# Kernel tuning notes

Measured on AMD Instinct MI355X. Metric: run time of the kernel, lower is better.

The kernel has to match this reference:

```python
import jax, jax.numpy as jnp
import numpy as np
from jax import lax

CONV3_NUM = 5
CONV1_NUM = 1
NEG_SLOPE = 0.2


def _leaky(x):
    return jnp.where(x >= 0, x, NEG_SLOPE * x)


def _per_sample_conv(x, k, b, pad):
    # x: [B,3,H,W], k: [B,3,3,kh,kw] (OIHW per sample), b: [B,3]
    def one(xi, ki, bi):
        y = lax.conv_general_dilated(
            xi[None], ki, (1, 1), ((pad, pad), (pad, pad)),
            dimension_numbers=("NCHW", "OIHW", "NCHW"))[0]
        return y + bi[:, None, None]
    return jax.vmap(one)(x, k, b)


def _conv3x3_block(x, feat):
    B = x.shape[0]
    k = feat[:, :81].reshape(B, 3, 3, 3, 3)
    b = feat[:, 81:84]
    return _leaky(x + _per_sample_conv(x, k, b, 1))


def _conv1x1_block(x, feat):
    B = x.shape[0]
    k = feat[:, :9].reshape(B, 3, 3, 1, 1)
    b = feat[:, 9:12]
    return _leaky(x + _per_sample_conv(x, k, b, 0))


def _att_map(f, h, w, xi):
    # f: [B,20]; h,w: [1,1,H,W]; xi: [B,1,H,W]  -> cubic trivariate polynomial
    c = lambda i: f[:, i][:, None, None, None]
    h2 = h * h; h3 = h2 * h
    w2 = w * w; w3 = w2 * w
    x2 = xi * xi; x3 = x2 * xi
    return (c(0) * h3 + c(1) * h2 * w + c(2) * h2 * xi + c(3) * h2
            + c(4) * h * w2 + c(5) * h * w * xi + c(6) * h * w
            + c(7) * h * x2 + c(8) * h * xi + c(9) * h
            + c(10) * w3 + c(11) * w2 * xi + c(12) * w2
            + c(13) * w * x2 + c(14) * w * xi + c(15) * w
            + c(16) * x3 + c(17) * x2 + c(18) * xi + c(19))


def setup_inputs() -> dict:
    key = jax.random.key(0)
    k1, k2, k3 = jax.random.split(key, 3)
    x = jax.random.normal(k1, (8, 3, 1024, 1024), dtype=jnp.float32)
    thumb_x = jax.random.normal(k2, (8, 3, 256, 256), dtype=jnp.float32)
    # meta() is an external CNN predicting per-sample params; we materialize its
    # output directly (scaled small for numerical stability of the conv stack).
    feature = jax.random.normal(k3, (8, 492), dtype=jnp.float32) * 0.05
    return {"x": x, "thumb_x": thumb_x, "feature": feature}


def reference(x, thumb_x, feature):
    B, _, H, W = x.shape
    residual = x
    for i in range(CONV3_NUM):
        x = _conv3x3_block(x, feature[:, i * 84:(i + 1) * 84])
    off = CONV3_NUM * 84
    for i in range(CONV1_NUM):
        x = _conv1x1_block(x, feature[:, off + i * 12:off + (i + 1) * 12])
    off = off + CONV1_NUM * 12
    x = residual + x
    dt = x.dtype
    h_mat = jnp.broadcast_to((jnp.arange(H, dtype=dt) / H)[None, None, :, None], (1, 1, H, W))
    w_mat = jnp.broadcast_to((jnp.arange(W, dtype=dt) / W)[None, None, None, :], (1, 1, H, W))
    atts = [_att_map(feature[:, off + 20 * c:off + 20 * (c + 1)], h_mat, w_mat, x[:, c:c + 1])
            for c in range(3)]
    att = jnp.concatenate(atts, axis=1)
    x = x * (1 + att)
    # location is None => thumbnail branch is skipped, thumb_x returned as-is
    return (x, thumb_x)
```

## Files before the change

kernel.cpp:

```cpp
#include <hip/hip_runtime.h>
#include <hip/hip_fp16.h>

typedef unsigned int uint;
typedef _Float16 h2 __attribute__((ext_vector_type(2)));


#define ROWS   42
#define W_U    26
#define W_REAL 23
#define CHP_U  (ROWS*W_U)
#define BUF_U  (3*CHP_U)

__device__ __forceinline__ h2   U2H(uint u) { return __builtin_bit_cast(h2, u); }
__device__ __forceinline__ uint H2U(h2 h)   { return __builtin_bit_cast(uint, h); }

__global__ void prep_weights(const float* __restrict__ feat, uint* __restrict__ wtab)
{
    const int b = blockIdx.x;
    const int t = threadIdx.x;
    float w = 0.f;
    bool valid = false;
    if (t < 405) {
        int l = t / 81, r = t % 81;
        int ic = r / 27; r %= 27;
        int ky = r / 9;  r %= 9;
        int oc = r / 3;
        int kx = r % 3;
        w = feat[b * 492 + l * 84 + ((oc * 3 + ic) * 3 + ky) * 3 + kx];
        valid = true;
    } else if (t < 420) {
        int i = t - 405;
        w = feat[b * 492 + (i / 3) * 84 + 81 + (i % 3)];
        valid = true;
    }
    if (valid) {
        _Float16 h = (_Float16)w;
        h2 hh = { h, h };
        wtab[b * 448 + t] = H2U(hh);
    }
}

__global__ __launch_bounds__(512, 8) void fused_net(
    const float* __restrict__ xin,
    const float* __restrict__ thumb,
    const float* __restrict__ feat,
    const uint*  __restrict__ wtab,
    float* __restrict__ out)
{
    const int tid = threadIdx.x;

    if (blockIdx.x == 32) {
        const int part = blockIdx.y + 32 * blockIdx.z;
        const float4* s4 = (const float4*)thumb;
        float4* d4 = (float4*)(out + 25165824ull);
        const int n4 = 1572864 / 4;
        for (int i = part * 512 + tid; i < n4; i += 256 * 512)
            d4[i] = s4[i];
        return;
    }

    const int gx0 = blockIdx.x * 32;
    const int gy0 = blockIdx.y * 32;
    const int b   = blockIdx.z;
    const bool edge = (gx0 == 0) | (gx0 == 992) | (gy0 == 0) | (gy0 == 992);
    const float* wf = feat + b * 492;
    const uint*  wt = wtab + b * 448;

    __shared__ uint lds[2 * BUF_U + 8];
    uint* b0 = lds;
    uint* b1 = lds + BUF_U + 4;

    const float* xb = xin + ((size_t)(b * 3) << 20);
    if (!edge) {
        for (int idx = tid; idx < 3 * ROWS * W_REAL; idx += 512) {
            int ch  = idx / (ROWS * W_REAL);
            int rem = idx - ch * (ROWS * W_REAL);
            int row = rem / W_REAL;
            int u   = rem - row * W_REAL;
            const float2 f = *(const float2*)(xb + ((size_t)ch << 20) +
                                              ((size_t)(gy0 - 5 + row) << 10) +
                                              (gx0 - 6 + 2 * u));
            b0[ch * CHP_U + row * W_U + u] =
                __builtin_bit_cast(uint, __builtin_amdgcn_cvt_pkrtz(f.x, f.y));
        }
    } else {
        for (int idx = tid; idx < 3 * ROWS * W_REAL; idx += 512) {
            int ch  = idx / (ROWS * W_REAL);
            int rem = idx - ch * (ROWS * W_REAL);
            int row = rem / W_REAL;
            int u   = rem - row * W_REAL;
            const int gy = gy0 - 5 + row;
            const int gx = gx0 - 6 + 2 * u;
            float2 f = {0.f, 0.f};
            if ((unsigned)gy < 1024u && (unsigned)gx < 1024u)
                f = *(const float2*)(xb + ((size_t)ch << 20) + ((size_t)gy << 10) + gx);
            b0[ch * CHP_U + row * W_U + u] =
                __builtin_bit_cast(uint, __builtin_amdgcn_cvt_pkrtz(f.x, f.y));
        }
    }
    __syncthreads();

    const int erow = tid >> 4;
    const int col2 = (tid & 15) << 1;
    const int ub   = (5 + erow) * W_U + 3 + (col2 >> 1);
    uint resu[3];
    #pragma unroll
    for (int ch = 0; ch < 3; ++ch) resu[ch] = b0[ch * CHP_U + ub];

    const h2 c02 = { (_Float16)0.2f, (_Float16)0.2f };

    #pragma unroll
    for (int l = 0; l < 5; ++l) {
        uint* sb = (l & 1) ? b1 : b0;
        uint* db = (l & 1) ? b0 : b1;
        const int S   = 40 - 2 * l;
        const int R   = S >> 1;
        const int xs  = (S + 3) >> 2;
        const int nst = R * xs;
        const int oy  = l + 1;
        const int EX  = (l + 2) & ~1;
        if (tid < nst) {
            const int r  = tid / xs;
            const int c  = tid - r * xs;
            const int y0 = oy + 2 * r;
            const int x0 = EX + 4 * c;
            const int bu = (x0 >> 1) - 1;

            h2 accA[2][3], accB[2][3];
            #pragma unroll
            for (int oc = 0; oc < 3; ++oc) {
                const h2 bi = U2H(wt[405 + l * 3 + oc]);
                accA[0][oc] = bi; accA[1][oc] = bi;
                accB[0][oc] = bi; accB[1][oc] = bi;
            }
            #pragma unroll
            for (int ic = 0; ic < 3; ++ic) {
                const int ai = ic * CHP_U + (y0 - 1) * W_U + bu;
                #pragma unroll
                for (int t = 0; t < 4; ++t) {
                    const int a = ai + t * W_U;
                    const uint u0 = sb[a], u1 = sb[a + 1], u2 = sb[a + 2], u3 = sb[a + 3];
                    const h2 X01 = U2H((u0 >> 16) | (u1 << 16));
                    const h2 C1  = U2H(u1);
                    const h2 X12 = U2H((u1 >> 16) | (u2 << 16));
                    const h2 C2  = U2H(u2);
                    const h2 X23 = U2H((u2 >> 16) | (u3 << 16));
                    #pragma unroll
                    for (int j = 0; j < 2; ++j) {
                        const int ky = t - j;
                        if (0 <= ky && ky <= 2) {
                            const int wb = l * 81 + (ic * 3 + ky) * 9;
                            #pragma unroll
                            for (int oc = 0; oc < 3; ++oc) {
                                const h2 w0 = U2H(wt[wb + oc * 3 + 0]);
                                const h2 w1 = U2H(wt[wb + oc * 3 + 1]);
                                const h2 w2 = U2H(wt[wb + oc * 3 + 2]);
                                accA[j][oc] = __builtin_elementwise_fma(w0, X01, accA[j][oc]);
                                accA[j][oc] = __builtin_elementwise_fma(w1, C1,  accA[j][oc]);
                                accA[j][oc] = __builtin_elementwise_fma(w2, X12, accA[j][oc]);
                                accB[j][oc] = __builtin_elementwise_fma(w0, X12, accB[j][oc]);
                                accB[j][oc] = __builtin_elementwise_fma(w1, C2,  accB[j][oc]);
                                accB[j][oc] = __builtin_elementwise_fma(w2, X23, accB[j][oc]);
                            }
                        }
                    }
                    if (t == 1) { accA[0][ic] += C1; accB[0][ic] += C2; }
                    if (t == 2) { accA[1][ic] += C1; accB[1][ic] += C2; }
                }
            }
            const int obase = y0 * W_U + (x0 >> 1);
            if (!edge) {
                #pragma unroll
                for (int j = 0; j < 2; ++j) {
                    #pragma unroll
                    for (int oc = 0; oc < 3; ++oc) {
                        h2 vA = accA[j][oc]; vA = __builtin_elementwise_max(vA, c02 * vA);
                        h2 vB = accB[j][oc]; vB = __builtin_elementwise_max(vB, c02 * vB);
                        db[oc * CHP_U + obase + j * W_U]     = H2U(vA);
                        db[oc * CHP_U + obase + j * W_U + 1] = H2U(vB);
                    }
                }
            } else {
                const int gy  = gy0 - 5 + y0;
                const int gxA = gx0 - 6 + x0;
                const uint mA0 = ((((unsigned)gxA       < 1024u) ? 0x0000ffffu : 0u) |
                                  (((unsigned)(gxA + 1) < 1024u) ? 0xffff0000u : 0u));
                const uint mB0 = ((((unsigned)(gxA + 2) < 1024u) ? 0x0000ffffu : 0u) |
                                  (((unsigned)(gxA + 3) < 1024u) ? 0xffff0000u : 0u));
                #pragma unroll
                for (int j = 0; j < 2; ++j) {
                    const uint mrow = ((unsigned)(gy + j) < 1024u) ? 0xffffffffu : 0u;
                    const uint mA = mrow & mA0, mB = mrow & mB0;
                    #pragma unroll
                    for (int oc = 0; oc < 3; ++oc) {
                        h2 vA = accA[j][oc]; vA = __builtin_elementwise_max(vA, c02 * vA);
                        h2 vB = accB[j][oc]; vB = __builtin_elementwise_max(vB, c02 * vB);
                        db[oc * CHP_U + obase + j * W_U]     = H2U(vA) & mA;
                        db[oc * CHP_U + obase + j * W_U + 1] = H2U(vB) & mB;
                    }
                }
            }
        }
        __syncthreads();
    }

    float x5f[3][2], resf[3][2];
    #pragma unroll
    for (int ch = 0; ch < 3; ++ch) {
        h2 hr = U2H(resu[ch]);
        resf[ch][0] = (float)hr.x; resf[ch][1] = (float)hr.y;
        h2 hx = U2H(b1[ch * CHP_U + ub]);
        x5f[ch][0] = (float)hx.x; x5f[ch][1] = (float)hx.y;
    }
    const int gy = gy0 + erow;
    const float h1 = (float)gy * (1.0f / 1024.0f);
    const float h2v = h1 * h1, h3 = h2v * h1;
    float* outb = out + ((size_t)(b * 3) << 20);
    float tmp[3][2];
    #pragma unroll
    for (int j = 0; j < 2; ++j) {
        const float wc = (float)(gx0 + col2 + j) * (1.0f / 1024.0f);
        const float w2 = wc * wc, w3 = w2 * wc;
        const float hw = h1 * wc, h2w = h2v * wc, hw2 = h1 * w2;
        #pragma unroll
        for (int oc = 0; oc < 3; ++oc) {
            float s = x5f[oc][j] + wf[429 + oc]
                    + wf[420 + oc * 3 + 0] * x5f[0][j]
                    + wf[420 + oc * 3 + 1] * x5f[1][j]
                    + wf[420 + oc * 3 + 2] * x5f[2][j];
            s = s >= 0.f ? s : 0.2f * s;
            const float xf = resf[oc][j] + s;
            const float x1 = xf, x2 = x1 * x1, x3 = x2 * x1;
            const float* cf = wf + 432 + oc * 20;
            float att =
                cf[0] * h3 + cf[1] * h2w + cf[2] * h2v * x1 + cf[3] * h2v +
                cf[4] * hw2 + cf[5] * hw * x1 + cf[6] * hw + cf[7] * h1 * x2 +
                cf[8] * h1 * x1 + cf[9] * h1 + cf[10] * w3 + cf[11] * w2 * x1 +
                cf[12] * w2 + cf[13] * wc * x2 + cf[14] * wc * x1 + cf[15] * wc +
                cf[16] * x3 + cf[17] * x2 + cf[18] * x1 + cf[19];
            tmp[oc][j] = xf * (1.f + att);
        }
    }
    #pragma unroll
    for (int oc = 0; oc < 3; ++oc) {
        float2 v = {tmp[oc][0], tmp[oc][1]};
        *(float2*)&outb[((size_t)oc << 20) + ((size_t)gy << 10) + (gx0 + col2)] = v;
    }
}

extern "C" void kernel_launch(void* const* d_in, const int* in_sizes, int n_in,
                              void* d_out, int out_size, void* d_ws, size_t ws_size,
                              hipStream_t stream) {
    const float* x     = (const float*)d_in[0];
    const float* thumb = (const float*)d_in[1];
    const float* feat  = (const float*)d_in[2];
    float* out = (float*)d_out;
    uint* wtab = (uint*)d_ws;

    prep_weights<<<dim3(8), 448, 0, stream>>>(feat, wtab);
    dim3 grid(33, 32, 8);
    fused_net<<<grid, 512, 0, stream>>>(x, thumb, feat, wtab, out);
}
```

Before: 301.4 us.

## Widen fused conv tile to 64 columns with fixed per-thread stencil mapping

Each block's output tile grows from 32x32 to 64 wide by 32 tall. The halo fraction per block falls, so less redundant halo compute and fewer global loads per output. Every layer now computes the full 40x72 region with a fixed thread-to-stencil mapping. LDS reads become 64-bit vector loads, and edge masks are computed once instead of branching per layer. The costs are a larger LDS footprint (occupancy hint lowered to 6), half as many blocks, and wasted computation on the shrinking interior region in later layers.

```diff
diff --git a/kernel.cpp b/kernel.cpp
--- a/kernel.cpp
+++ b/kernel.cpp
@@ -6,8 +6,8 @@
 
 
 #define ROWS   42
-#define W_U    26
-#define W_REAL 23
+#define W_U    42
+#define W_REAL 38
 #define CHP_U  (ROWS*W_U)
 #define BUF_U  (3*CHP_U)
 
@@ -40,7 +40,7 @@
     }
 }
 
-__global__ __launch_bounds__(512, 8) void fused_net(
+__global__ __launch_bounds__(512, 6) void fused_net(
     const float* __restrict__ xin,
     const float* __restrict__ thumb,
     const float* __restrict__ feat,
@@ -49,7 +49,7 @@
 {
     const int tid = threadIdx.x;
 
-    if (blockIdx.x == 32) {
+    if (blockIdx.x == 16) {
         const int part = blockIdx.y + 32 * blockIdx.z;
         const float4* s4 = (const float4*)thumb;
         float4* d4 = (float4*)(out + 25165824ull);
@@ -59,14 +59,14 @@
         return;
     }
 
-    const int gx0 = blockIdx.x * 32;
+    const int gx0 = blockIdx.x * 64;
     const int gy0 = blockIdx.y * 32;
     const int b   = blockIdx.z;
-    const bool edge = (gx0 == 0) | (gx0 == 992) | (gy0 == 0) | (gy0 == 992);
+    const bool edge = (gx0 == 0) | (gx0 == 960) | (gy0 == 0) | (gy0 == 992);
     const float* wf = feat + b * 492;
     const uint*  wt = wtab + b * 448;
 
-    __shared__ uint lds[2 * BUF_U + 8];
+    __shared__ __align__(16) uint lds[2 * BUF_U + 8];
     uint* b0 = lds;
     uint* b1 = lds + BUF_U + 4;
 
@@ -100,32 +100,46 @@
     }
     __syncthreads();
 
-    const int erow = tid >> 4;
-    const int col2 = (tid & 15) << 1;
-    const int ub   = (5 + erow) * W_U + 3 + (col2 >> 1);
-    uint resu[3];
+    const int er  = tid >> 5;
+    const int uc  = tid & 31;
+    const int ub0 = (5 + er) * W_U + 3 + uc;
+    const int ub1 = ub0 + 16 * W_U;
+    uint resu[2][3];
     #pragma unroll
-    for (int ch = 0; ch < 3; ++ch) resu[ch] = b0[ch * CHP_U + ub];
+    for (int ch = 0; ch < 3; ++ch) {
+        resu[0][ch] = b0[ch * CHP_U + ub0];
+        resu[1][ch] = b0[ch * CHP_U + ub1];
+    }
+
+    const int cr = tid / 18;
+    const int cc = tid - cr * 18;
+    const int y0 = 1 + 2 * cr;
+    const int x0 = 2 + 4 * cc;
+    uint mA[2] = {~0u, ~0u}, mB[2] = {~0u, ~0u};
+    if (edge) {
+        const int gyA = gy0 - 5 + y0;
+        const int gxA = gx0 - 6 + x0;
+        const uint mA0 = ((((unsigned)gxA       < 1024u) ? 0x0000ffffu : 0u) |
+                          (((unsigned)(gxA + 1) < 1024u) ? 0xffff0000u : 0u));
+        const uint mB0 = ((((unsigned)(gxA + 2) < 1024u) ? 0x0000ffffu : 0u) |
+                          (((unsigned)(gxA + 3) < 1024u) ? 0xffff0000u : 0u));
+        #pragma unroll
+        for (int j = 0; j < 2; ++j) {
+            const uint mr = ((unsigned)(gyA + j) < 1024u) ? ~0u : 0u;
+            mA[j] = mA0 & mr;
+            mB[j] = mB0 & mr;
+        }
+    }
 
     const h2 c02 = { (_Float16)0.2f, (_Float16)0.2f };
 
     #pragma unroll
     for (int l = 0; l < 5; ++l) {
-        uint* sb = (l & 1) ? b1 : b0;
-        uint* db = (l & 1) ? b0 : b1;
-        const int S   = 40 - 2 * l;
-        const int R   = S >> 1;
-        const int xs  = (S + 3) >> 2;
-        const int nst = R * xs;
-        const int oy  = l + 1;
-        const int EX  = (l + 2) & ~1;
-        if (tid < nst) {
-            const int r  = tid / xs;
-            const int c  = tid - r * xs;
-            const int y0 = oy + 2 * r;
-            const int x0 = EX + 4 * c;
-            const int bu = (x0 >> 1) - 1;
-
+        const uint* sb = (l & 1) ? b1 : b0;
+        uint*       db = (l & 1) ? b0 : b1;
+        if (tid < 360) {
+            const uint* tb = sb + (y0 - 1) * W_U + 2 * cc;
+            uint*       ob = db + y0 * W_U + 1 + 2 * cc;
             h2 accA[2][3], accB[2][3];
             #pragma unroll
             for (int oc = 0; oc < 3; ++oc) {
@@ -135,11 +149,11 @@
             }
             #pragma unroll
             for (int ic = 0; ic < 3; ++ic) {
-                const int ai = ic * CHP_U + (y0 - 1) * W_U + bu;
                 #pragma unroll
                 for (int t = 0; t < 4; ++t) {
-                    const int a = ai + t * W_U;
-                    const uint u0 = sb[a], u1 = sb[a + 1], u2 = sb[a + 2], u3 = sb[a + 3];
+                    const uint2 P = *(const uint2*)(tb + ic * CHP_U + t * W_U);
+                    const uint2 Q = *(const uint2*)(tb + ic * CHP_U + t * W_U + 2);
+                    const uint u0 = P.x, u1 = P.y, u2 = Q.x, u3 = Q.y;
                     const h2 X01 = U2H((u0 >> 16) | (u1 << 16));
                     const h2 C1  = U2H(u1);
                     const h2 X12 = U2H((u1 >> 16) | (u2 << 16));
@@ -164,87 +178,69 @@
                             }
                         }
                     }
-                    if (t == 1) { accA[0][ic] += C1; accB[0][ic] += C2; }
-                    if (t == 2) { accA[1][ic] += C1; accB[1][ic] += C2; }
+                    if (t == 1) { accA[0][ic] = accA[0][ic] + C1; accB[0][ic] = accB[0][ic] + C2; }
+                    if (t == 2) { accA[1][ic] = accA[1][ic] + C1; accB[1][ic] = accB[1][ic] + C2; }
                 }
             }
-            const int obase = y0 * W_U + (x0 >> 1);
-            if (!edge) {
+            #pragma unroll
+            for (int j = 0; j < 2; ++j) {
                 #pragma unroll
-                for (int j = 0; j < 2; ++j) {
-                    #pragma unroll
-                    for (int oc = 0; oc < 3; ++oc) {
-                        h2 vA = accA[j][oc]; vA = __builtin_elementwise_max(vA, c02 * vA);
-                        h2 vB = accB[j][oc]; vB = __builtin_elementwise_max(vB, c02 * vB);
-                        db[oc * CHP_U + obase + j * W_U]     = H2U(vA);
-                        db[oc * CHP_U + obase + j * W_U + 1] = H2U(vB);
-                    }
+                for (int oc = 0; oc < 3; ++oc) {
+                    h2 vA = accA[j][oc]; vA = __builtin_elementwise_max(vA, c02 * vA);
+                    h2 vB = accB[j][oc]; vB = __builtin_elementwise_max(vB, c02 * vB);
+                    ob[oc * CHP_U + j * W_U]     = H2U(vA) & mA[j];
+                    ob[oc * CHP_U + j * W_U + 1] = H2U(vB) & mB[j];
                 }
-            } else {
-                const int gy  = gy0 - 5 + y0;
-                const int gxA = gx0 - 6 + x0;
-                const uint mA0 = ((((unsigned)gxA       < 1024u) ? 0x0000ffffu : 0u) |
-                                  (((unsigned)(gxA + 1) < 1024u) ? 0xffff0000u : 0u));
-                const uint mB0 = ((((unsigned)(gxA + 2) < 1024u) ? 0x0000ffffu : 0u) |
-                                  (((unsigned)(gxA + 3) < 1024u) ? 0xffff0000u : 0u));
-                #pragma unroll
-                for (int j = 0; j < 2; ++j) {
-                    const uint mrow = ((unsigned)(gy + j) < 1024u) ? 0xffffffffu : 0u;
-                    const uint mA = mrow & mA0, mB = mrow & mB0;
-                    #pragma unroll
-                    for (int oc = 0; oc < 3; ++oc) {
-                        h2 vA = accA[j][oc]; vA = __builtin_elementwise_max(vA, c02 * vA);
-                        h2 vB = accB[j][oc]; vB = __builtin_elementwise_max(vB, c02 * vB);
-                        db[oc * CHP_U + obase + j * W_U]     = H2U(vA) & mA;
-                        db[oc * CHP_U + obase + j * W_U + 1] = H2U(vB) & mB;
-                    }
-                }
             }
         }
         __syncthreads();
     }
 
-    float x5f[3][2], resf[3][2];
+    float* outb = out + ((size_t)(b * 3) << 20);
     #pragma unroll
-    for (int ch = 0; ch < 3; ++ch) {
-        h2 hr = U2H(resu[ch]);
-        resf[ch][0] = (float)hr.x; resf[ch][1] = (float)hr.y;
-        h2 hx = U2H(b1[ch * CHP_U + ub]);
-        x5f[ch][0] = (float)hx.x; x5f[ch][1] = (float)hx.y;
-    }
-    const int gy = gy0 + erow;
-    const float h1 = (float)gy * (1.0f / 1024.0f);
-    const float h2v = h1 * h1, h3 = h2v * h1;
-    float* outb = out + ((size_t)(b * 3) << 20);
-    float tmp[3][2];
-    #pragma unroll
-    for (int j = 0; j < 2; ++j) {
-        const float wc = (float)(gx0 + col2 + j) * (1.0f / 1024.0f);
-        const float w2 = wc * wc, w3 = w2 * wc;
-        const float hw = h1 * wc, h2w = h2v * wc, hw2 = h1 * w2;
+    for (int rr = 0; rr < 2; ++rr) {
+        const int ub = rr ? ub1 : ub0;
+        const int gy = gy0 + er + 16 * rr;
+        float x5f[3][2], resf[3][2];
+        #pragma unroll
+        for (int ch = 0; ch < 3; ++ch) {
+            h2 hr = U2H(resu[rr][ch]);
+            resf[ch][0] = (float)hr.x; resf[ch][1] = (float)hr.y;
+            h2 hx = U2H(b1[ch * CHP_U + ub]);
+            x5f[ch][0] = (float)hx.x; x5f[ch][1] = (float)hx.y;
+        }
+        const float h1 = (float)gy * (1.0f / 1024.0f);
+        const float h2v = h1 * h1, h3 = h2v * h1;
+        float tmp[3][2];
+        #pragma unroll
+        for (int j = 0; j < 2; ++j) {
+            const float wc = (float)(gx0 + 2 * uc + j) * (1.0f / 1024.0f);
+            const float w2 = wc * wc, w3 = w2 * wc;
+            const float hw = h1 * wc, h2w = h2v * wc, hw2 = h1 * w2;
+            #pragma unroll
+            for (int oc = 0; oc < 3; ++oc) {
+                float s = x5f[oc][j] + wf[429 + oc]
+                        + wf[420 + oc * 3 + 0] * x5f[0][j]
+                        + wf[420 + oc * 3 + 1] * x5f[1][j]
+                        + wf[420 + oc * 3 + 2] * x5f[2][j];
+                s = s >= 0.f ? s : 0.2f * s;
+                const float xf = resf[oc][j] + s;
+                const float x1 = xf, x2 = x1 * x1, x3 = x2 * x1;
+                const float* cf = wf + 432 + oc * 20;
+                float att =
+                    cf[0] * h3 + cf[1] * h2w + cf[2] * h2v * x1 + cf[3] * h2v +
+                    cf[4] * hw2 + cf[5] * hw * x1 + cf[6] * hw + cf[7] * h1 * x2 +
+                    cf[8] * h1 * x1 + cf[9] * h1 + cf[10] * w3 + cf[11] * w2 * x1 +
+                    cf[12] * w2 + cf[13] * wc * x2 + cf[14] * wc * x1 + cf[15] * wc +
+                    cf[16] * x3 + cf[17] * x2 + cf[18] * x1 + cf[19];
+                tmp[oc][j] = xf * (1.f + att);
+            }
+        }
         #pragma unroll
         for (int oc = 0; oc < 3; ++oc) {
-            float s = x5f[oc][j] + wf[429 + oc]
-                    + wf[420 + oc * 3 + 0] * x5f[0][j]
-                    + wf[420 + oc * 3 + 1] * x5f[1][j]
-                    + wf[420 + oc * 3 + 2] * x5f[2][j];
-            s = s >= 0.f ? s : 0.2f * s;
-            const float xf = resf[oc][j] + s;
-            const float x1 = xf, x2 = x1 * x1, x3 = x2 * x1;
-            const float* cf = wf + 432 + oc * 20;
-            float att =
-                cf[0] * h3 + cf[1] * h2w + cf[2] * h2v * x1 + cf[3] * h2v +
-                cf[4] * hw2 + cf[5] * hw * x1 + cf[6] * hw + cf[7] * h1 * x2 +
-                cf[8] * h1 * x1 + cf[9] * h1 + cf[10] * w3 + cf[11] * w2 * x1 +
-                cf[12] * w2 + cf[13] * wc * x2 + cf[14] * wc * x1 + cf[15] * wc +
-                cf[16] * x3 + cf[17] * x2 + cf[18] * x1 + cf[19];
-            tmp[oc][j] = xf * (1.f + att);
-        }
-    }
-    #pragma unroll
-    for (int oc = 0; oc < 3; ++oc) {
-        float2 v = {tmp[oc][0], tmp[oc][1]};
-        *(float2*)&outb[((size_t)oc << 20) + ((size_t)gy << 10) + (gx0 + col2)] = v;
+            float2 v = {tmp[oc][0], tmp[oc][1]};
+            *(float2*)&outb[((size_t)oc << 20) + ((size_t)gy << 10) + (gx0 + 2 * uc)] = v;
+        }
     }
 }
 
@@ -258,6 +254,6 @@
     uint* wtab = (uint*)d_ws;
 
     prep_weights<<<dim3(8), 448, 0, stream>>>(feat, wtab);
-    dim3 grid(33, 32, 8);
+    dim3 grid(17, 32, 8);
     fused_net<<<grid, 512, 0, stream>>>(x, thumb, feat, wtab, out);
 }
```

After: 302.4 us. No clear change (+0.3%).
